# Performance work log

Hardware: AMD Instinct MI355X
Metric: run time of the kernel (lower is better)

Reference implementation:

```python
import jax, jax.numpy as jnp
import numpy as np

B, L, DIM = 4, 2048, 256
NSETS, PP, POSP, LTMP = 4, 4, 16, 16
PI = float(np.pi)


def setup_inputs() -> dict:
    key = jax.random.key(0)
    ks = jax.random.split(key, 8)
    d = DIM
    return {
        "x": jax.random.normal(ks[0], (B, L, d), jnp.float32),
        "key_proj": jax.random.normal(ks[1], (d, NSETS * PP), jnp.float32) / np.sqrt(d),
        "query_proj": jax.random.normal(ks[2], (d, NSETS * PP), jnp.float32) / np.sqrt(d),
        "ltm_key_proj": jax.random.normal(ks[3], (3 * d, LTMP), jnp.float32) / np.sqrt(3 * d),
        "pos_freqs": jnp.exp(jnp.arange(POSP, dtype=jnp.float32) * (-np.log(10000.0) / POSP)),
        "w_value": jax.random.normal(ks[4], (d, d), jnp.float32) / np.sqrt(d),
        "b_value": jnp.zeros(d, jnp.float32),
        "w_ltm_val": jax.random.normal(ks[5], (d, d), jnp.float32) / np.sqrt(d),
        "b_ltm_val": jnp.zeros(d, jnp.float32),
        "ln_gamma": jnp.ones(d, jnp.float32),
        "ln_beta": jnp.zeros(d, jnp.float32),
        "w_out": jax.random.normal(ks[6], (d, d), jnp.float32) / np.sqrt(d),
        "b_out": jnp.zeros(d, jnp.float32),
        "set_weights": jnp.ones(NSETS, jnp.float32),
        "pos_weight": jnp.ones(1, jnp.float32),
        "surprise_scale": jnp.array(5.0, jnp.float32),
        "surprise_bias": jnp.array(0.0, jnp.float32),
        "resonance_scale": jnp.array(5.0, jnp.float32),
        "resonance_threshold": jnp.array(0.3, jnp.float32),
        "ltm_weight": jnp.array(0.5, jnp.float32),
        "ltm_binding_memory": jnp.zeros((LTMP, d), jnp.complex64),
        "ltm_count": jnp.array(0.0, jnp.float32),
    }


def reference(x, key_proj, query_proj, ltm_key_proj, pos_freqs, w_value, b_value,
              w_ltm_val, b_ltm_val, ln_gamma, ln_beta, w_out, b_out, set_weights,
              pos_weight, surprise_scale, surprise_bias, resonance_scale,
              resonance_threshold, ltm_weight, ltm_binding_memory, ltm_count):
    Bx, Lx, D = x.shape
    # phasor encodings
    key_ph = jnp.exp(1j * (jnp.tanh(x @ key_proj) * PI)).reshape(Bx, Lx, NSETS, PP)
    qry_ph = jnp.exp(1j * (jnp.tanh(x @ query_proj) * PI)).reshape(Bx, Lx, NSETS, PP)
    V_real = x @ w_value + b_value
    weights = jax.nn.softmax(set_weights)
    # joint (cross-bank) phasors
    jk = jnp.prod(key_ph, axis=2)   # [B,L,PP]
    jq = jnp.prod(qry_ph, axis=2)
    # exclusive cumsum of joint keys -> resonance-based surprise write gate
    km = jnp.concatenate([jnp.zeros_like(jk[:, :1]), jnp.cumsum(jk[:, :-1], axis=1)], axis=1)
    rmag = jnp.abs(km * jnp.conj(jq)).mean(-1, keepdims=True)
    posf = jnp.maximum(jnp.arange(Lx, dtype=jnp.float32), 1.0)
    nres = rmag / jnp.sqrt(posf)[None, :, None]
    sc = jnp.clip(resonance_scale, 1.0, 20.0)
    th = jnp.clip(resonance_threshold, 0.1, 0.9)
    surprise = 0.5 * (1.0 - jnp.tanh(sc * (nres - th)))
    gate = jax.nn.sigmoid(surprise_scale * (surprise - 0.5) + surprise_bias)
    Vg = (V_real * gate).astype(jnp.complex64)
    # cross-bank holographic memory (joint key binding)
    cross = jnp.real((jnp.cumsum(jk[..., None] * Vg[:, :, None, :], axis=1)
                      * jnp.conj(jq)[..., None]).sum(2))
    # per-bank holographic memory over all planes
    bound_all = key_ph[..., None] * Vg[:, :, None, None, :]            # [B,L,S,P,D]
    mem_all = jnp.cumsum(bound_all.reshape(Bx, Lx, NSETS * PP, D), axis=1)
    mem_all = mem_all.reshape(Bx, Lx, NSETS, PP, D)
    per_bank = jnp.real((mem_all * jnp.conj(qry_ph)[..., None]).sum(3))  # [B,L,S,D]
    total = (per_bank * weights[None, None, :, None]).sum(2)
    total = (total + cross) / (NSETS + 1.0)
    # positional phasor memory (ungated V)
    pos_ph = jnp.exp(1j * (jnp.arange(Lx, dtype=jnp.float32)[:, None] * pos_freqs * 2.0 * PI))  # [L,P]
    Vc = V_real.astype(jnp.complex64)
    ret_pos = jnp.real((jnp.cumsum(pos_ph[None, :, :, None] * Vc[:, :, None, :], axis=1)
                        * jnp.conj(pos_ph)[None, :, :, None]).sum(2))
    total = 0.5 * total + 0.5 * (jax.nn.sigmoid(pos_weight) * ret_pos)  # fixed_gate = 0.5
    # LTM retrieval from persistent binding memory (detached buffers)
    p1 = jnp.arange(1, Lx + 1, dtype=jnp.float32)[None, :, None]
    rm = jnp.cumsum(x, axis=1) / p1
    rv = jnp.cumsum(x * x, axis=1) / p1 - rm * rm
    rs = jnp.sqrt(jnp.clip(rv, 1e-8, None))
    ltm_ph = jnp.exp(1j * (jnp.tanh(jnp.concatenate([x, rm, rs], -1) @ ltm_key_proj) * PI))  # [B,L,LTMP]
    pers = jnp.real((ltm_binding_memory[None, None] * jnp.conj(ltm_ph)[..., None]).sum(2))
    pnorm = jnp.sqrt(jnp.maximum(ltm_count, 1.0) * LTMP)
    total = total + jax.nn.sigmoid(ltm_weight) * (pers / pnorm)
    # output: LayerNorm + Linear on normalized retrieval, residual
    nrm = jnp.sqrt(jnp.arange(1, Lx + 1, dtype=jnp.float32) * PP)[None, :, None]
    h = total / nrm
    mu = h.mean(-1, keepdims=True)
    var = ((h - mu) ** 2).mean(-1, keepdims=True)
    hn = (h - mu) / jnp.sqrt(var + 1e-5) * ln_gamma + ln_beta
    return x + hn @ w_out + b_out
```

## Files before the change

kernel.cpp:

```cpp
#include <hip/hip_runtime.h>
#include <math.h>

#define B 4
#define L 2048
#define D 256
#define POSP 16
#define LTMP 16
#define T 64
#define C 32
#define F 72
#define PI_F 3.14159274101257324f
#define TWO_PI_D 6.283185307179586476925286766559

__global__ __launch_bounds__(256) void pos_kernel(const float* __restrict__ pos_freqs,
                                                  const float* __restrict__ lkp,
                                                  float* __restrict__ posc,
                                                  float* __restrict__ poss,
                                                  float* __restrict__ Wt) {
    int idx = blockIdx.x * 256 + threadIdx.x;
    if (idx < L * POSP) {
        int t = idx >> 4, p = idx & 15;
        float a = (float)t * pos_freqs[p];
        float th = (a * 2.0f) * PI_F;
        double r = fmod((double)th, TWO_PI_D);
        posc[idx] = (float)cos(r);
        poss[idx] = (float)sin(r);
    } else {
        int i2 = idx - L * POSP;
        if (i2 < 16 * 768) {
            int p = i2 / 768, j = i2 - p * 768;
            Wt[i2] = lkp[j * 16 + p];
        }
    }
}

__global__ __launch_bounds__(256) void featurize_kernel(
    const float* __restrict__ x, const float* __restrict__ key_proj,
    const float* __restrict__ query_proj, const float* __restrict__ w_value,
    const float* __restrict__ b_value, const float* __restrict__ set_weights,
    float* __restrict__ V, float* __restrict__ fk, float* __restrict__ fq,
    float* __restrict__ partial) {
    int cg = blockIdx.x;
    int rc = blockIdx.y;
    int b  = blockIdx.z;
    int row0 = rc * 64;
    int tid = threadIdx.x;
    __shared__ float xs[2][32][74];
    __shared__ float ws[2][32][84];
    __shared__ float zbuf[64][20];
    __shared__ float jkv[64][9];
    const bool has_proj = (cg < 2);
    const float* proj = (cg == 0) ? key_proj : query_proj;
    int rg = tid >> 4, cgi = tid & 15;
    int r0 = rg * 4, c0 = cgi * 4;
    int prow = tid >> 2, pc4 = tid & 3;
    float acc[4][4], accp[4];
#pragma unroll
    for (int i = 0; i < 4; i++) {
#pragma unroll
        for (int e = 0; e < 4; e++) acc[i][e] = 0.f;
        accp[i] = 0.f;
    }
    int rrA = tid >> 3, k4A = tid & 7;
    int jA = tid >> 4, c4A = tid & 15;
    float4 xr0, xr1, wr0, wr1, prr;

#define ISSUE_LOADS(kb_)                                                            \
    {                                                                               \
        xr0 = *(const float4*)(x + ((size_t)(b * L + row0 + rrA)) * D + (kb_) + k4A * 4);      \
        xr1 = *(const float4*)(x + ((size_t)(b * L + row0 + 32 + rrA)) * D + (kb_) + k4A * 4); \
        wr0 = *(const float4*)(w_value + (size_t)((kb_) + jA) * D + cg * 64 + c4A * 4);        \
        wr1 = *(const float4*)(w_value + (size_t)((kb_) + 16 + jA) * D + cg * 64 + c4A * 4);   \
        if (has_proj && tid < 128)                                                  \
            prr = *(const float4*)(proj + (size_t)((kb_) + (tid >> 2)) * 16 + (tid & 3) * 4);  \
    }
#define WRITE_LDS(bi)                                                               \
    {                                                                               \
        const float* xp0 = (const float*)&xr0;                                      \
        const float* xp1 = (const float*)&xr1;                                      \
        _Pragma("unroll")                                                           \
        for (int u = 0; u < 4; u++) {                                               \
            xs[bi][k4A * 4 + u][rrA] = xp0[u];                                      \
            xs[bi][k4A * 4 + u][32 + rrA] = xp1[u];                                 \
        }                                                                           \
        *(float4*)&ws[bi][jA][c4A * 4] = wr0;                                       \
        *(float4*)&ws[bi][16 + jA][c4A * 4] = wr1;                                  \
        if (has_proj && tid < 128)                                                  \
            *(float4*)&ws[bi][tid >> 2][64 + (tid & 3) * 4] = prr;                  \
    }

    ISSUE_LOADS(0);
    WRITE_LDS(0);
    __syncthreads();
    for (int kc = 0; kc < 8; kc++) {
        if (kc < 7) ISSUE_LOADS((kc + 1) * 32);
        int bi = kc & 1;
#pragma unroll 8
        for (int j = 0; j < 32; j++) {
            float2 xlo = *(float2*)&xs[bi][j][r0];
            float2 xhi = *(float2*)&xs[bi][j][r0 + 2];
            float4 wv = *(float4*)&ws[bi][j][c0];
            acc[0][0] += xlo.x * wv.x; acc[0][1] += xlo.x * wv.y; acc[0][2] += xlo.x * wv.z; acc[0][3] += xlo.x * wv.w;
            acc[1][0] += xlo.y * wv.x; acc[1][1] += xlo.y * wv.y; acc[1][2] += xlo.y * wv.z; acc[1][3] += xlo.y * wv.w;
            acc[2][0] += xhi.x * wv.x; acc[2][1] += xhi.x * wv.y; acc[2][2] += xhi.x * wv.z; acc[2][3] += xhi.x * wv.w;
            acc[3][0] += xhi.y * wv.x; acc[3][1] += xhi.y * wv.y; acc[3][2] += xhi.y * wv.z; acc[3][3] += xhi.y * wv.w;
            if (has_proj) {
                float xp = xs[bi][j][prow];
                float4 wp = *(float4*)&ws[bi][j][64 + pc4 * 4];
                accp[0] += xp * wp.x; accp[1] += xp * wp.y;
                accp[2] += xp * wp.z; accp[3] += xp * wp.w;
            }
        }
        if (kc < 7) WRITE_LDS((kc + 1) & 1);
        __syncthreads();
    }
#undef ISSUE_LOADS
#undef WRITE_LDS

    {
        int d0 = cg * 64 + c0;
        float4 bv = *(const float4*)(b_value + d0);
#pragma unroll
        for (int i = 0; i < 4; i++) {
            size_t o = ((size_t)(b * L + row0 + r0 + i)) * D + d0;
            *(float4*)(V + o) = make_float4(acc[i][0] + bv.x, acc[i][1] + bv.y,
                                            acc[i][2] + bv.z, acc[i][3] + bv.w);
        }
    }
    if (!has_proj) return;
#pragma unroll
    for (int e = 0; e < 4; e++) zbuf[prow][pc4 * 4 + e] = tanhf(accp[e]) * PI_F;
    __syncthreads();
    {
        int tt = tid >> 2, q = tid & 3;
        size_t bt = (size_t)(b * L + row0 + tt);
        if (cg == 0) {
            float* fp = fk + bt * 40;
#pragma unroll
            for (int e = 0; e < 4; e++) {
                int col = q * 4 + e;
                float si, co; sincosf(zbuf[tt][col], &si, &co);
                fp[2 * col] = co; fp[2 * col + 1] = si;
            }
            float zs = zbuf[tt][q] + zbuf[tt][4 + q] + zbuf[tt][8 + q] + zbuf[tt][12 + q];
            float si, co; sincosf(zs, &si, &co);
            fp[32 + 2 * q] = co; fp[33 + 2 * q] = si;
            jkv[tt][2 * q] = co; jkv[tt][2 * q + 1] = si;
        } else {
            float sw0 = set_weights[0], sw1 = set_weights[1], sw2 = set_weights[2], sw3 = set_weights[3];
            float mx = fmaxf(fmaxf(sw0, sw1), fmaxf(sw2, sw3));
            float e0 = expf(sw0 - mx), e1 = expf(sw1 - mx), e2 = expf(sw2 - mx), e3 = expf(sw3 - mx);
            float esum = e0 + e1 + e2 + e3;
            float wsoft[4] = {e0 / esum, e1 / esum, e2 / esum, e3 / esum};
            float* fp = fq + bt * 40;
#pragma unroll
            for (int e = 0; e < 4; e++) {
                int col = q * 4 + e;
                float si, co; sincosf(zbuf[tt][col], &si, &co);
                float sc = 0.1f * wsoft[col >> 2];
                fp[2 * col] = sc * co; fp[2 * col + 1] = sc * si;
            }
            float zs = zbuf[tt][q] + zbuf[tt][4 + q] + zbuf[tt][8 + q] + zbuf[tt][12 + q];
            float si, co; sincosf(zs, &si, &co);
            fp[32 + 2 * q] = 0.1f * co; fp[33 + 2 * q] = 0.1f * si;
        }
    }
    __syncthreads();
    if (cg == 0) {
        int h = tid >> 7, idxr = tid & 127;
        int rr2 = idxr >> 3, ch = idxr & 7;
#pragma unroll
        for (int s2 = 16; s2 >= 1; s2 >>= 1) {
            if (rr2 < s2) jkv[h * 32 + rr2][ch] += jkv[h * 32 + rr2 + s2][ch];
            __syncthreads();
        }
        if (rr2 == 0) partial[((size_t)(b * 64 + rc * 2 + h)) * 8 + ch] = jkv[h * 32][ch];
    }
}

__global__ __launch_bounds__(512) void gs_scan_kernel(const float* __restrict__ partial,
                                                      float* __restrict__ chunkoff) {
    int b = blockIdx.x;
    int tid = threadIdx.x;
    int c = tid >> 3, ch = tid & 7;
    __shared__ float sc_[64][9];
    float own = partial[((size_t)(b * 64 + c)) * 8 + ch];
    sc_[c][ch] = own;
    __syncthreads();
    for (int off = 1; off < 64; off <<= 1) {
        float v = 0.f;
        if (c >= off) v = sc_[c - off][ch];
        __syncthreads();
        if (c >= off) sc_[c][ch] += v;
        __syncthreads();
    }
    chunkoff[((size_t)(b * 64 + c)) * 8 + ch] = sc_[c][ch] - own;
}

__global__ __launch_bounds__(256) void gs_apply_kernel(
    float* __restrict__ fk, const float* __restrict__ chunkoff,
    const float* __restrict__ surprise_scale, const float* __restrict__ surprise_bias,
    const float* __restrict__ resonance_scale, const float* __restrict__ resonance_threshold) {
    int rc = blockIdx.x, b = blockIdx.y;
    int tid = threadIdx.x;
    int t = tid >> 3, ch = tid & 7;
    __shared__ float sc_[32][9];
    __shared__ float gbuf[32];
    float* fp = fk + ((size_t)(b * L + rc * 32 + t)) * 40;
    float own = fp[32 + ch];
    sc_[t][ch] = own;
    __syncthreads();
    for (int off = 1; off < 32; off <<= 1) {
        float v = 0.f;
        if (t >= off) v = sc_[t - off][ch];
        __syncthreads();
        if (t >= off) sc_[t][ch] += v;
        __syncthreads();
    }
    float run = chunkoff[((size_t)(b * 64 + rc)) * 8 + ch] + sc_[t][ch] - own;
    __syncthreads();
    sc_[t][ch] = run;
    __syncthreads();
    if (tid < 32) {
        int tg = rc * 32 + tid;
        float r0 = sc_[tid][0], r1 = sc_[tid][1], r2 = sc_[tid][2], r3 = sc_[tid][3];
        float r4 = sc_[tid][4], r5 = sc_[tid][5], r6 = sc_[tid][6], r7 = sc_[tid][7];
        float rmag = 0.25f * (sqrtf(r0 * r0 + r1 * r1) + sqrtf(r2 * r2 + r3 * r3) +
                              sqrtf(r4 * r4 + r5 * r5) + sqrtf(r6 * r6 + r7 * r7));
        float scv = fminf(fmaxf(resonance_scale[0], 1.f), 20.f);
        float thv = fminf(fmaxf(resonance_threshold[0], 0.1f), 0.9f);
        float nres = rmag / sqrtf(fmaxf((float)tg, 1.0f));
        float surprise = 0.5f * (1.0f - tanhf(scv * (nres - thv)));
        gbuf[tid] = 1.0f / (1.0f + expf(-(surprise_scale[0] * (surprise - 0.5f) + surprise_bias[0])));
    }
    __syncthreads();
    float gv = gbuf[t];
#pragma unroll
    for (int e = 0; e < 5; e++) fp[ch * 5 + e] *= gv;
}

__global__ __launch_bounds__(256) void stats16_kernel(const float* __restrict__ x,
                                                      float* __restrict__ Sx16,
                                                      float* __restrict__ Sxx16) {
    int s = blockIdx.x, b = blockIdx.y;
    int d = threadIdx.x;
    float sx = 0.f, sxx = 0.f;
#pragma unroll
    for (int k = 0; k < 16; k++) {
        float v = x[((size_t)(b * L + s * 16 + k)) * D + d];
        sx += v; sxx += v * v;
    }
    Sx16[((size_t)(b * 128 + s)) * D + d] = sx;
    Sxx16[((size_t)(b * 128 + s)) * D + d] = sxx;
}

__global__ __launch_bounds__(256) void ltm_z_kernel(
    const float* __restrict__ x, const float* __restrict__ Sx16,
    const float* __restrict__ Sxx16, const float* __restrict__ Wt,
    float* __restrict__ czsz) {
    int s = blockIdx.x, b = blockIdx.y;
    int tid = threadIdx.x;
    __shared__ float xs[16][260], rms[16][260], rss[16][260];
    float a0 = 0.f, a1 = 0.f, a2 = 0.f, a3 = 0.f;
    float c0 = 0.f, c1 = 0.f, c2 = 0.f, c3 = 0.f;
    int sp = 0;
    for (; sp + 4 <= s; sp += 4) {
        a0 += Sx16[((size_t)(b * 128 + sp)) * D + tid];
        a1 += Sx16[((size_t)(b * 128 + sp + 1)) * D + tid];
        a2 += Sx16[((size_t)(b * 128 + sp + 2)) * D + tid];
        a3 += Sx16[((size_t)(b * 128 + sp + 3)) * D + tid];
        c0 += Sxx16[((size_t)(b * 128 + sp)) * D + tid];
        c1 += Sxx16[((size_t)(b * 128 + sp + 1)) * D + tid];
        c2 += Sxx16[((size_t)(b * 128 + sp + 2)) * D + tid];
        c3 += Sxx16[((size_t)(b * 128 + sp + 3)) * D + tid];
    }
    for (; sp < s; sp++) {
        a0 += Sx16[((size_t)(b * 128 + sp)) * D + tid];
        c0 += Sxx16[((size_t)(b * 128 + sp)) * D + tid];
    }
    float runx = (a0 + a1) + (a2 + a3), runxx = (c0 + c1) + (c2 + c3);
    for (int k = 0; k < 16; k++) {
        int tg = s * 16 + k;
        float xv = x[((size_t)(b * L + tg)) * D + tid];
        runx += xv; runxx += xv * xv;
        float n = (float)(tg + 1);
        float rm = runx / n;
        float rv = runxx / n - rm * rm;
        xs[k][tid] = xv; rms[k][tid] = rm;
        rss[k][tid] = sqrtf(fmaxf(rv, 1e-8f));
    }
    __syncthreads();
    int tl = tid & 15, p = tid >> 4;
    const float* W0 = Wt + p * 768;
    float u0 = 0.f, u1 = 0.f, u2 = 0.f;
#pragma unroll 4
    for (int j4 = 0; j4 < 64; j4++) {
        float4 xv = *(float4*)&xs[tl][j4 * 4];
        float4 wx = *(const float4*)(W0 + j4 * 4);
        float4 rv = *(float4*)&rms[tl][j4 * 4];
        float4 wr = *(const float4*)(W0 + 256 + j4 * 4);
        float4 sv = *(float4*)&rss[tl][j4 * 4];
        float4 wz = *(const float4*)(W0 + 512 + j4 * 4);
        u0 += xv.x * wx.x + xv.y * wx.y + xv.z * wx.z + xv.w * wx.w;
        u1 += rv.x * wr.x + rv.y * wr.y + rv.z * wr.z + rv.w * wr.w;
        u2 += sv.x * wz.x + sv.y * wz.y + sv.z * wz.z + sv.w * wz.w;
    }
    float z = tanhf(u0 + u1 + u2) * PI_F;
    float si, co; sincosf(z, &si, &co);
    int tg = s * 16 + tl;
    czsz[((size_t)(b * L + tg)) * 32 + p] = co;
    czsz[((size_t)(b * L + tg)) * 32 + 16 + p] = si;
}

__global__ __launch_bounds__(256) void outer_sums_kernel(
    const float* __restrict__ V, const float* __restrict__ fk,
    const float* __restrict__ posc, const float* __restrict__ poss,
    float* __restrict__ Sh) {
    int g = blockIdx.x >> 1, h = blockIdx.x & 1;
    int c = blockIdx.y;
    int b = blockIdx.z;
    int tid = threadIdx.x;
    __shared__ float Fk[32][40];
    int F0 = g * 36;
    {
        int t = tid >> 3, q = tid & 7;
        int tg = c * T + h * 32 + t;
#pragma unroll
        for (int e = 0; e < 5; e++) {
            int fl = q * 5 + e;
            float v = 0.f;
            if (fl < 36) {
                int Fi = F0 + fl;
                if (Fi < 40) v = fk[((size_t)(b * L + tg)) * 40 + Fi];
                else {
                    int pf = Fi - 40;
                    v = (pf & 1) ? poss[tg * POSP + (pf >> 1)] : posc[tg * POSP + (pf >> 1)];
                }
            }
            Fk[t][fl] = v;
        }
    }
    __syncthreads();
    float acc[36];
#pragma unroll
    for (int f = 0; f < 36; f++) acc[f] = 0.f;
    for (int t = 0; t < 32; t++) {
        float v = V[((size_t)(b * L + c * T + h * 32 + t)) * D + tid];
#pragma unroll
        for (int f4 = 0; f4 < 9; f4++) {
            float4 fkv = *(float4*)&Fk[t][f4 * 4];
            acc[f4 * 4 + 0] += fkv.x * v;
            acc[f4 * 4 + 1] += fkv.y * v;
            acc[f4 * 4 + 2] += fkv.z * v;
            acc[f4 * 4 + 3] += fkv.w * v;
        }
    }
    for (int f = 0; f < 36; f++)
        Sh[((((size_t)(b * C + c)) * 2 + h) * F + F0 + f) * D + tid] = acc[f];
}

__global__ __launch_bounds__(256) void prefix_kernel(const float* __restrict__ Sh,
                                                     float* __restrict__ S) {
    int bf = blockIdx.x;
    int b = bf / F, f = bf % F;
    int d = threadIdx.x;
    float v0[C], v1[C];
#pragma unroll
    for (int c = 0; c < C; c++) {
        v0[c] = Sh[((((size_t)(b * C + c)) * 2 + 0) * F + f) * D + d];
        v1[c] = Sh[((((size_t)(b * C + c)) * 2 + 1) * F + f) * D + d];
    }
    float run = 0.f;
#pragma unroll
    for (int c = 0; c < C; c++) {
        S[(((size_t)(b * C + c)) * F + f) * D + d] = run;
        run += v0[c] + v1[c];
    }
}

__global__ __launch_bounds__(256) void intra_kernel(
    const float* __restrict__ V, float* __restrict__ ret,
    const float* __restrict__ fk, const float* __restrict__ fq,
    const float* __restrict__ posc, const float* __restrict__ poss,
    const float* __restrict__ Mexc, const float* __restrict__ pos_weight) {
    int tg = blockIdx.x >> 1, dh = blockIdx.x & 1;
    int c = blockIdx.y, b = blockIdx.z;
    int tid = threadIdx.x;
    int t0 = tg * 16;
    __shared__ float Fk[64][76];
    __shared__ float Fq[16][76];
    __shared__ float As[16][68];
    float posq = 0.5f / (1.0f + expf(-pos_weight[0]));
#pragma unroll
    for (int e = 0; e < 18; e++) {
        int idx = e * 256 + tid;
        int r = idx / 72, f = idx - r * 72;
        int tgl = c * T + r;
        float v;
        if (f < 40) v = fk[((size_t)(b * L + tgl)) * 40 + f];
        else { int pf = f - 40; v = (pf & 1) ? poss[tgl * POSP + (pf >> 1)] : posc[tgl * POSP + (pf >> 1)]; }
        Fk[r][f] = v;
    }
#pragma unroll
    for (int e = 0; e < 5; e++) {
        int idx = e * 256 + tid;
        if (idx < 1152) {
            int r = idx / 72, f = idx - r * 72;
            int tgl = c * T + t0 + r;
            float v;
            if (f < 40) v = fq[((size_t)(b * L + tgl)) * 40 + f];
            else { int pf = f - 40; v = posq * ((pf & 1) ? poss[tgl * POSP + (pf >> 1)] : posc[tgl * POSP + (pf >> 1)]); }
            Fq[r][f] = v;
        }
    }
    __syncthreads();
    {
        int r = tid >> 4, k0 = (tid & 15) * 4;
        int tglob = t0 + r;
#pragma unroll
        for (int j = 0; j < 4; j++) {
            int k = k0 + j;
            float a = 0.f;
            if (k <= tglob) {
#pragma unroll
                for (int f4 = 0; f4 < 18; f4++) {
                    float4 q = *(float4*)&Fq[r][f4 * 4];
                    float4 kk = *(float4*)&Fk[k][f4 * 4];
                    a += q.x * kk.x + q.y * kk.y + q.z * kk.z + q.w * kk.w;
                }
            }
            As[r][k] = a;
        }
    }
    __syncthreads();
    int dl = tid & 127, rowg = tid >> 7;
    int d = dh * 128 + dl;
    int r0 = rowg * 8;
    float acc[8];
#pragma unroll
    for (int i = 0; i < 8; i++) acc[i] = 0.f;
    const float* Mp = Mexc + (((size_t)(b * C + c)) * F) * D + d;
#pragma unroll 8
    for (int f = 0; f < F; f++) {
        float m = Mp[(size_t)f * D];
#pragma unroll
        for (int i = 0; i < 8; i++) acc[i] += Fq[r0 + i][f] * m;
    }
    const float* Vp = V + ((size_t)(b * L + c * T)) * D + d;
    int kmax = t0 + 16;
#pragma unroll 8
    for (int k = 0; k < kmax; k++) {
        float v = Vp[(size_t)k * D];
#pragma unroll
        for (int i = 0; i < 8; i++) acc[i] += As[r0 + i][k] * v;
    }
    float* Rp = ret + ((size_t)(b * L + c * T + t0 + r0)) * D + d;
#pragma unroll
    for (int i = 0; i < 8; i++) Rp[(size_t)i * D] = acc[i];
}

__global__ __launch_bounds__(256) void hprep_kernel(
    const float* __restrict__ retp, const float* __restrict__ czsz,
    const float* __restrict__ ltm_mem, const float* __restrict__ ltm_count,
    const float* __restrict__ ltm_weight, const float* __restrict__ ln_gamma,
    const float* __restrict__ ln_beta, float* __restrict__ hn) {
    int rc = blockIdx.x;
    int b  = blockIdx.y;
    int row0 = rc * 16;
    int tid = threadIdx.x;
    __shared__ float hb[16][260];
    __shared__ float cs[16][33];
    __shared__ float part1[16][17], part2[16][17];
    __shared__ float mu[16], rsig[16];
    float lsig = 1.f / (1.f + expf(-ltm_weight[0]));
    float pnorm = sqrtf(fmaxf(ltm_count[0], 1.f) * (float)LTMP);
    float lcoef = lsig / pnorm;
    float Mre[16], Mim[16];
#pragma unroll
    for (int p = 0; p < 16; p++) {
        Mre[p] = ltm_mem[(p * D + tid) * 2];
        Mim[p] = ltm_mem[(p * D + tid) * 2 + 1];
    }
    float gam = ln_gamma[tid], bet = ln_beta[tid];
#pragma unroll
    for (int e = 0; e < 2; e++) {
        int idx = e * 256 + tid;
        int t = idx >> 5, q = idx & 31;
        cs[t][q] = czsz[((size_t)(b * L + row0 + t)) * 32 + q];
    }
    __syncthreads();
#pragma unroll 4
    for (int t = 0; t < 16; t++) {
        int tg = row0 + t;
        float pers = 0.f;
#pragma unroll
        for (int p = 0; p < 16; p++) pers += Mre[p] * cs[t][p] + Mim[p] * cs[t][16 + p];
        float rv = retp[((size_t)(b * L + tg)) * D + tid];
        hb[t][tid] = (rv + lcoef * pers) / (2.0f * sqrtf((float)(tg + 1)));
    }
    __syncthreads();
    {
        int row = tid & 15, e = tid >> 4;
        float s1 = 0.f, s2 = 0.f;
#pragma unroll
        for (int k = 0; k < 16; k++) {
            float v = hb[row][e + 16 * k];
            s1 += v; s2 += v * v;
        }
        part1[row][e] = s1; part2[row][e] = s2;
    }
    __syncthreads();
    if (tid < 16) {
        float s1 = 0.f, s2 = 0.f;
#pragma unroll
        for (int e = 0; e < 16; e++) { s1 += part1[tid][e]; s2 += part2[tid][e]; }
        float m = s1 / 256.f;
        mu[tid] = m;
        rsig[tid] = rsqrtf(fmaxf(s2 / 256.f - m * m, 0.f) + 1e-5f);
    }
    __syncthreads();
#pragma unroll 4
    for (int t = 0; t < 16; t++)
        hn[((size_t)(b * L + row0 + t)) * D + tid] =
            (hb[t][tid] - mu[t]) * rsig[t] * gam + bet;
}

__global__ __launch_bounds__(256) void gemm_out_kernel(
    const float* __restrict__ hn, const float* __restrict__ w_out,
    const float* __restrict__ b_out, const float* __restrict__ x,
    float* __restrict__ out) {
    int cg = blockIdx.x;
    int rc = blockIdx.y;
    int b  = blockIdx.z;
    int row0 = rc * 64;
    int tid = threadIdx.x;
    __shared__ float hs[2][32][74];
    __shared__ float wo[2][32][68];
    int rg = tid >> 4, cgi = tid & 15;
    int r0 = rg * 4, c0 = cgi * 4;
    float acc[4][4];
#pragma unroll
    for (int i = 0; i < 4; i++)
#pragma unroll
        for (int e = 0; e < 4; e++) acc[i][e] = 0.f;
    int rrA = tid >> 3, k4A = tid & 7;
    int jA = tid >> 4, c4A = tid & 15;
    float4 hr0, hr1, wr0, wr1;

#define ISSUE_LOADS(kb_)                                                            \
    {                                                                               \
        hr0 = *(const float4*)(hn + ((size_t)(b * L + row0 + rrA)) * D + (kb_) + k4A * 4);      \
        hr1 = *(const float4*)(hn + ((size_t)(b * L + row0 + 32 + rrA)) * D + (kb_) + k4A * 4); \
        wr0 = *(const float4*)(w_out + (size_t)((kb_) + jA) * D + cg * 64 + c4A * 4);           \
        wr1 = *(const float4*)(w_out + (size_t)((kb_) + 16 + jA) * D + cg * 64 + c4A * 4);      \
    }
#define WRITE_LDS(bi)                                                               \
    {                                                                               \
        const float* hp0 = (const float*)&hr0;                                      \
        const float* hp1 = (const float*)&hr1;                                      \
        _Pragma("unroll")                                                           \
        for (int u = 0; u < 4; u++) {                                               \
            hs[bi][k4A * 4 + u][rrA] = hp0[u];                                      \
            hs[bi][k4A * 4 + u][32 + rrA] = hp1[u];                                 \
        }                                                                           \
        *(float4*)&wo[bi][jA][c4A * 4] = wr0;                                       \
        *(float4*)&wo[bi][16 + jA][c4A * 4] = wr1;                                  \
    }

    ISSUE_LOADS(0);
    WRITE_LDS(0);
    __syncthreads();
    for (int kc = 0; kc < 8; kc++) {
        if (kc < 7) ISSUE_LOADS((kc + 1) * 32);
        int bi = kc & 1;
#pragma unroll 8
        for (int j = 0; j < 32; j++) {
            float2 xlo = *(float2*)&hs[bi][j][r0];
            float2 xhi = *(float2*)&hs[bi][j][r0 + 2];
            float4 wv = *(float4*)&wo[bi][j][c0];
            acc[0][0] += xlo.x * wv.x; acc[0][1] += xlo.x * wv.y; acc[0][2] += xlo.x * wv.z; acc[0][3] += xlo.x * wv.w;
            acc[1][0] += xlo.y * wv.x; acc[1][1] += xlo.y * wv.y; acc[1][2] += xlo.y * wv.z; acc[1][3] += xlo.y * wv.w;
            acc[2][0] += xhi.x * wv.x; acc[2][1] += xhi.x * wv.y; acc[2][2] += xhi.x * wv.z; acc[2][3] += xhi.x * wv.w;
            acc[3][0] += xhi.y * wv.x; acc[3][1] += xhi.y * wv.y; acc[3][2] += xhi.y * wv.z; acc[3][3] += xhi.y * wv.w;
        }
        if (kc < 7) WRITE_LDS((kc + 1) & 1);
        __syncthreads();
    }
#undef ISSUE_LOADS
#undef WRITE_LDS
    {
        int d0 = cg * 64 + c0;
        float4 bo = *(const float4*)(b_out + d0);
#pragma unroll
        for (int i = 0; i < 4; i++) {
            size_t o = ((size_t)(b * L + row0 + r0 + i)) * D + d0;
            float4 xa = *(const float4*)(x + o);
            *(float4*)(out + o) = make_float4(xa.x + acc[i][0] + bo.x, xa.y + acc[i][1] + bo.y,
                                              xa.z + acc[i][2] + bo.z, xa.w + acc[i][3] + bo.w);
        }
    }
}

extern "C" void kernel_launch(void* const* d_in, const int* in_sizes, int n_in,
                              void* d_out, int out_size, void* d_ws, size_t ws_size,
                              hipStream_t stream) {
    (void)in_sizes; (void)n_in; (void)out_size; (void)ws_size;
    const float* x            = (const float*)d_in[0];
    const float* key_proj     = (const float*)d_in[1];
    const float* query_proj   = (const float*)d_in[2];
    const float* ltm_key_proj = (const float*)d_in[3];
    const float* pos_freqs    = (const float*)d_in[4];
    const float* w_value      = (const float*)d_in[5];
    const float* b_value      = (const float*)d_in[6];
    const float* ln_gamma     = (const float*)d_in[9];
    const float* ln_beta      = (const float*)d_in[10];
    const float* w_out        = (const float*)d_in[11];
    const float* b_out        = (const float*)d_in[12];
    const float* set_weights  = (const float*)d_in[13];
    const float* pos_weight   = (const float*)d_in[14];
    const float* surprise_scale      = (const float*)d_in[15];
    const float* surprise_bias       = (const float*)d_in[16];
    const float* resonance_scale     = (const float*)d_in[17];
    const float* resonance_threshold = (const float*)d_in[18];
    const float* ltm_weight   = (const float*)d_in[19];
    const float* ltm_mem      = (const float*)d_in[20];
    const float* ltm_count    = (const float*)d_in[21];
    float* out = (float*)d_out;

    float* ws = (float*)d_ws;
    size_t off = 0;
    float* V     = ws + off; off += (size_t)B * L * D;
    float* ret   = ws + off; off += (size_t)B * L * D;
    float* fk    = ws + off; off += (size_t)B * L * 40;
    float* fq    = ws + off; off += (size_t)B * L * 40;
    float* posc  = ws + off; off += (size_t)L * POSP;
    float* poss  = ws + off; off += (size_t)L * POSP;
    float* Sx16  = ws + off; off += (size_t)B * 128 * D;
    float* Sxx16 = ws + off; off += (size_t)B * 128 * D;
    float* czsz  = ws + off; off += (size_t)B * L * 32;
    float* Sh    = ws + off; off += (size_t)B * C * 2 * F * D;
    float* S     = ws + off; off += (size_t)B * C * F * D;
    float* partial  = ws + off; off += (size_t)B * 64 * 8;
    float* chunkoff = ws + off; off += (size_t)B * 64 * 8;
    float* Wt    = ws + off; off += (size_t)16 * 768;
    float* hn = V;

    pos_kernel<<<dim3(176), 256, 0, stream>>>(pos_freqs, ltm_key_proj, posc, poss, Wt);
    featurize_kernel<<<dim3(4, 32, B), 256, 0, stream>>>(x, key_proj, query_proj, w_value,
                                                         b_value, set_weights, V, fk, fq, partial);
    gs_scan_kernel<<<dim3(B), 512, 0, stream>>>(partial, chunkoff);
    gs_apply_kernel<<<dim3(64, B), 256, 0, stream>>>(fk, chunkoff, surprise_scale, surprise_bias,
                                                     resonance_scale, resonance_threshold);
    stats16_kernel<<<dim3(128, B), 256, 0, stream>>>(x, Sx16, Sxx16);
    ltm_z_kernel<<<dim3(128, B), 256, 0, stream>>>(x, Sx16, Sxx16, Wt, czsz);
    outer_sums_kernel<<<dim3(4, C, B), 256, 0, stream>>>(V, fk, posc, poss, Sh);
    prefix_kernel<<<dim3(B * F), 256, 0, stream>>>(Sh, S);
    intra_kernel<<<dim3(8, C, B), 256, 0, stream>>>(V, ret, fk, fq, posc, poss, S, pos_weight);
    hprep_kernel<<<dim3(128, B), 256, 0, stream>>>(ret, czsz, ltm_mem, ltm_count, ltm_weight,
                                                   ln_gamma, ln_beta, hn);
    gemm_out_kernel<<<dim3(4, 32, B), 256, 0, stream>>>(hn, w_out, b_out, x, out);
}
```

Measured before the change: 248.8 us.

## Fuse gate scan into one kernel and merge hprep LayerNorm into intra kernel

Replaces the three-step gated-surprise path (partial reduce in featurize, gs_scan, gs_apply) with a single 1024-thread-per-batch gate_kernel that scans joint key phasors across the whole sequence and rescales fk. Separately folds hprep (LTM retrieval, normalization, LayerNorm) into intra_kernel so each block computes all 256 channels for 16 rows, avoiding writing and re-reading the ret buffer. This removes two launches and a full B*L*D round trip. In exchange, intra now runs half as many blocks with 16 accumulators per thread, and the gate scan runs on only four blocks with a long serial log-step scan.

```diff
diff --git a/kernel.cpp b/kernel.cpp
--- a/kernel.cpp
+++ b/kernel.cpp
@@ -38,8 +38,7 @@
     const float* __restrict__ x, const float* __restrict__ key_proj,
     const float* __restrict__ query_proj, const float* __restrict__ w_value,
     const float* __restrict__ b_value, const float* __restrict__ set_weights,
-    float* __restrict__ V, float* __restrict__ fk, float* __restrict__ fq,
-    float* __restrict__ partial) {
+    float* __restrict__ V, float* __restrict__ fk, float* __restrict__ fq) {
     int cg = blockIdx.x;
     int rc = blockIdx.y;
     int b  = blockIdx.z;
@@ -48,7 +47,6 @@
     __shared__ float xs[2][32][74];
     __shared__ float ws[2][32][84];
     __shared__ float zbuf[64][20];
-    __shared__ float jkv[64][9];
     const bool has_proj = (cg < 2);
     const float* proj = (cg == 0) ? key_proj : query_proj;
     int rg = tid >> 4, cgi = tid & 15;
@@ -145,7 +143,6 @@
             float zs = zbuf[tt][q] + zbuf[tt][4 + q] + zbuf[tt][8 + q] + zbuf[tt][12 + q];
             float si, co; sincosf(zs, &si, &co);
             fp[32 + 2 * q] = co; fp[33 + 2 * q] = si;
-            jkv[tt][2 * q] = co; jkv[tt][2 * q + 1] = si;
         } else {
             float sw0 = set_weights[0], sw1 = set_weights[1], sw2 = set_weights[2], sw3 = set_weights[3];
             float mx = fmaxf(fmaxf(sw0, sw1), fmaxf(sw2, sw3));
@@ -165,78 +162,61 @@
             fp[32 + 2 * q] = 0.1f * co; fp[33 + 2 * q] = 0.1f * si;
         }
     }
-    __syncthreads();
-    if (cg == 0) {
-        int h = tid >> 7, idxr = tid & 127;
-        int rr2 = idxr >> 3, ch = idxr & 7;
-#pragma unroll
-        for (int s2 = 16; s2 >= 1; s2 >>= 1) {
-            if (rr2 < s2) jkv[h * 32 + rr2][ch] += jkv[h * 32 + rr2 + s2][ch];
-            __syncthreads();
-        }
-        if (rr2 == 0) partial[((size_t)(b * 64 + rc * 2 + h)) * 8 + ch] = jkv[h * 32][ch];
-    }
-}
-
-__global__ __launch_bounds__(512) void gs_scan_kernel(const float* __restrict__ partial,
-                                                      float* __restrict__ chunkoff) {
+}
+
+__global__ __launch_bounds__(1024) void gate_kernel(
+    float* __restrict__ fk,
+    const float* __restrict__ surprise_scale, const float* __restrict__ surprise_bias,
+    const float* __restrict__ resonance_scale, const float* __restrict__ resonance_threshold) {
     int b = blockIdx.x;
     int tid = threadIdx.x;
-    int c = tid >> 3, ch = tid & 7;
-    __shared__ float sc_[64][9];
-    float own = partial[((size_t)(b * 64 + c)) * 8 + ch];
-    sc_[c][ch] = own;
-    __syncthreads();
-    for (int off = 1; off < 64; off <<= 1) {
-        float v = 0.f;
-        if (c >= off) v = sc_[c - off][ch];
+    __shared__ float scan[1024][8];
+    float j0[8], j1[8], tot[8];
+    float* fp0 = fk + ((size_t)(b * L + tid * 2)) * 40;
+    float* fp1 = fk + ((size_t)(b * L + tid * 2 + 1)) * 40;
+#pragma unroll
+    for (int q = 0; q < 8; q++) {
+        j0[q] = fp0[32 + q];
+        j1[q] = fp1[32 + q];
+        tot[q] = j0[q] + j1[q];
+        scan[tid][q] = tot[q];
+    }
+    __syncthreads();
+    for (int off = 1; off < 1024; off <<= 1) {
+        float tmp[8];
+        if (tid >= off) {
+#pragma unroll
+            for (int q = 0; q < 8; q++) tmp[q] = scan[tid - off][q];
+        }
         __syncthreads();
-        if (c >= off) sc_[c][ch] += v;
+        if (tid >= off) {
+#pragma unroll
+            for (int q = 0; q < 8; q++) scan[tid][q] += tmp[q];
+        }
         __syncthreads();
     }
-    chunkoff[((size_t)(b * 64 + c)) * 8 + ch] = sc_[c][ch] - own;
-}
-
-__global__ __launch_bounds__(256) void gs_apply_kernel(
-    float* __restrict__ fk, const float* __restrict__ chunkoff,
-    const float* __restrict__ surprise_scale, const float* __restrict__ surprise_bias,
-    const float* __restrict__ resonance_scale, const float* __restrict__ resonance_threshold) {
-    int rc = blockIdx.x, b = blockIdx.y;
-    int tid = threadIdx.x;
-    int t = tid >> 3, ch = tid & 7;
-    __shared__ float sc_[32][9];
-    __shared__ float gbuf[32];
-    float* fp = fk + ((size_t)(b * L + rc * 32 + t)) * 40;
-    float own = fp[32 + ch];
-    sc_[t][ch] = own;
-    __syncthreads();
-    for (int off = 1; off < 32; off <<= 1) {
-        float v = 0.f;
-        if (t >= off) v = sc_[t - off][ch];
-        __syncthreads();
-        if (t >= off) sc_[t][ch] += v;
-        __syncthreads();
-    }
-    float run = chunkoff[((size_t)(b * 64 + rc)) * 8 + ch] + sc_[t][ch] - own;
-    __syncthreads();
-    sc_[t][ch] = run;
-    __syncthreads();
-    if (tid < 32) {
-        int tg = rc * 32 + tid;
-        float r0 = sc_[tid][0], r1 = sc_[tid][1], r2 = sc_[tid][2], r3 = sc_[tid][3];
-        float r4 = sc_[tid][4], r5 = sc_[tid][5], r6 = sc_[tid][6], r7 = sc_[tid][7];
-        float rmag = 0.25f * (sqrtf(r0 * r0 + r1 * r1) + sqrtf(r2 * r2 + r3 * r3) +
-                              sqrtf(r4 * r4 + r5 * r5) + sqrtf(r6 * r6 + r7 * r7));
-        float scv = fminf(fmaxf(resonance_scale[0], 1.f), 20.f);
-        float thv = fminf(fmaxf(resonance_threshold[0], 0.1f), 0.9f);
-        float nres = rmag / sqrtf(fmaxf((float)tg, 1.0f));
+    float run[8];
+#pragma unroll
+    for (int q = 0; q < 8; q++) run[q] = scan[tid][q] - tot[q];
+    float ss = surprise_scale[0], sb = surprise_bias[0];
+    float scv = fminf(fmaxf(resonance_scale[0], 1.f), 20.f);
+    float thv = fminf(fmaxf(resonance_threshold[0], 0.1f), 0.9f);
+#pragma unroll
+    for (int k = 0; k < 2; k++) {
+        int t = tid * 2 + k;
+        float* fp = k ? fp1 : fp0;
+        float rmag = 0.25f * (sqrtf(run[0] * run[0] + run[1] * run[1]) +
+                              sqrtf(run[2] * run[2] + run[3] * run[3]) +
+                              sqrtf(run[4] * run[4] + run[5] * run[5]) +
+                              sqrtf(run[6] * run[6] + run[7] * run[7]));
+        float nres = rmag / sqrtf(fmaxf((float)t, 1.0f));
         float surprise = 0.5f * (1.0f - tanhf(scv * (nres - thv)));
-        gbuf[tid] = 1.0f / (1.0f + expf(-(surprise_scale[0] * (surprise - 0.5f) + surprise_bias[0])));
-    }
-    __syncthreads();
-    float gv = gbuf[t];
-#pragma unroll
-    for (int e = 0; e < 5; e++) fp[ch * 5 + e] *= gv;
+        float gate = 1.0f / (1.0f + expf(-(ss * (surprise - 0.5f) + sb)));
+#pragma unroll
+        for (int q = 0; q < 8; q++) run[q] += (k ? j1[q] : j0[q]);
+#pragma unroll
+        for (int q = 0; q < 40; q++) fp[q] *= gate;
+    }
 }
 
 __global__ __launch_bounds__(256) void stats16_kernel(const float* __restrict__ x,
@@ -379,17 +359,26 @@
 }
 
 __global__ __launch_bounds__(256) void intra_kernel(
-    const float* __restrict__ V, float* __restrict__ ret,
+    const float* __restrict__ V, float* __restrict__ hn,
     const float* __restrict__ fk, const float* __restrict__ fq,
     const float* __restrict__ posc, const float* __restrict__ poss,
-    const float* __restrict__ Mexc, const float* __restrict__ pos_weight) {
-    int tg = blockIdx.x >> 1, dh = blockIdx.x & 1;
-    int c = blockIdx.y, b = blockIdx.z;
+    const float* __restrict__ Mexc, const float* __restrict__ pos_weight,
+    const float* __restrict__ czsz, const float* __restrict__ ltm_mem,
+    const float* __restrict__ ltm_count, const float* __restrict__ ltm_weight,
+    const float* __restrict__ ln_gamma, const float* __restrict__ ln_beta) {
+    int tg = blockIdx.x, c = blockIdx.y, b = blockIdx.z;
     int tid = threadIdx.x;
     int t0 = tg * 16;
-    __shared__ float Fk[64][76];
-    __shared__ float Fq[16][76];
-    __shared__ float As[16][68];
+    __shared__ float smem[8384];
+    float (*Fk)[76] = (float(*)[76])smem;
+    float (*Fq)[76] = (float(*)[76])(smem + 4864);
+    float (*As)[68] = (float(*)[68])(smem + 6080);
+    float (*cs)[33]  = (float(*)[33])(smem + 7168);
+    float (*part1)[17] = (float(*)[17])(smem + 7696);
+    float (*part2)[17] = (float(*)[17])(smem + 7968);
+    float* mu   = smem + 8240;
+    float* rsig = smem + 8256;
+    float (*hb)[260] = (float(*)[260])smem;
     float posq = 0.5f / (1.0f + expf(-pos_weight[0]));
 #pragma unroll
     for (int e = 0; e < 18; e++) {
@@ -413,6 +402,15 @@
             Fq[r][f] = v;
         }
     }
+    {
+        int idx2 = tid;
+#pragma unroll
+        for (int e = 0; e < 2; e++) {
+            int idx = e * 256 + idx2;
+            int t = idx >> 5, q = idx & 31;
+            cs[t][q] = czsz[((size_t)(b * L + c * T + t0 + t)) * 32 + q];
+        }
+    }
     __syncthreads();
     {
         int r = tid >> 4, k0 = (tid & 15) * 4;
@@ -433,18 +431,16 @@
         }
     }
     __syncthreads();
-    int dl = tid & 127, rowg = tid >> 7;
-    int d = dh * 128 + dl;
-    int r0 = rowg * 8;
-    float acc[8];
-#pragma unroll
-    for (int i = 0; i < 8; i++) acc[i] = 0.f;
+    int d = tid;
+    float acc[16];
+#pragma unroll
+    for (int i = 0; i < 16; i++) acc[i] = 0.f;
     const float* Mp = Mexc + (((size_t)(b * C + c)) * F) * D + d;
 #pragma unroll 8
     for (int f = 0; f < F; f++) {
         float m = Mp[(size_t)f * D];
 #pragma unroll
-        for (int i = 0; i < 8; i++) acc[i] += Fq[r0 + i][f] * m;
+        for (int i = 0; i < 16; i++) acc[i] += Fq[i][f] * m;
     }
     const float* Vp = V + ((size_t)(b * L + c * T)) * D + d;
     int kmax = t0 + 16;
@@ -452,52 +448,28 @@
     for (int k = 0; k < kmax; k++) {
         float v = Vp[(size_t)k * D];
 #pragma unroll
-        for (int i = 0; i < 8; i++) acc[i] += As[r0 + i][k] * v;
-    }
-    float* Rp = ret + ((size_t)(b * L + c * T + t0 + r0)) * D + d;
-#pragma unroll
-    for (int i = 0; i < 8; i++) Rp[(size_t)i * D] = acc[i];
-}
-
-__global__ __launch_bounds__(256) void hprep_kernel(
-    const float* __restrict__ retp, const float* __restrict__ czsz,
-    const float* __restrict__ ltm_mem, const float* __restrict__ ltm_count,
-    const float* __restrict__ ltm_weight, const float* __restrict__ ln_gamma,
-    const float* __restrict__ ln_beta, float* __restrict__ hn) {
-    int rc = blockIdx.x;
-    int b  = blockIdx.y;
-    int row0 = rc * 16;
-    int tid = threadIdx.x;
-    __shared__ float hb[16][260];
-    __shared__ float cs[16][33];
-    __shared__ float part1[16][17], part2[16][17];
-    __shared__ float mu[16], rsig[16];
+        for (int i = 0; i < 16; i++) acc[i] += As[i][k] * v;
+    }
     float lsig = 1.f / (1.f + expf(-ltm_weight[0]));
     float pnorm = sqrtf(fmaxf(ltm_count[0], 1.f) * (float)LTMP);
     float lcoef = lsig / pnorm;
     float Mre[16], Mim[16];
 #pragma unroll
     for (int p = 0; p < 16; p++) {
-        Mre[p] = ltm_mem[(p * D + tid) * 2];
-        Mim[p] = ltm_mem[(p * D + tid) * 2 + 1];
-    }
-    float gam = ln_gamma[tid], bet = ln_beta[tid];
-#pragma unroll
-    for (int e = 0; e < 2; e++) {
-        int idx = e * 256 + tid;
-        int t = idx >> 5, q = idx & 31;
-        cs[t][q] = czsz[((size_t)(b * L + row0 + t)) * 32 + q];
-    }
-    __syncthreads();
-#pragma unroll 4
-    for (int t = 0; t < 16; t++) {
-        int tg = row0 + t;
+        Mre[p] = ltm_mem[(p * D + d) * 2];
+        Mim[p] = ltm_mem[(p * D + d) * 2 + 1];
+    }
+#pragma unroll
+    for (int i = 0; i < 16; i++) {
         float pers = 0.f;
 #pragma unroll
-        for (int p = 0; p < 16; p++) pers += Mre[p] * cs[t][p] + Mim[p] * cs[t][16 + p];
-        float rv = retp[((size_t)(b * L + tg)) * D + tid];
-        hb[t][tid] = (rv + lcoef * pers) / (2.0f * sqrtf((float)(tg + 1)));
-    }
+        for (int p = 0; p < 16; p++) pers += Mre[p] * cs[i][p] + Mim[p] * cs[i][16 + p];
+        int tgl = c * T + t0 + i;
+        acc[i] = (acc[i] + lcoef * pers) / (2.0f * sqrtf((float)(tgl + 1)));
+    }
+    __syncthreads();
+#pragma unroll
+    for (int i = 0; i < 16; i++) hb[i][d] = acc[i];
     __syncthreads();
     {
         int row = tid & 15, e = tid >> 4;
@@ -519,10 +491,11 @@
         rsig[tid] = rsqrtf(fmaxf(s2 / 256.f - m * m, 0.f) + 1e-5f);
     }
     __syncthreads();
-#pragma unroll 4
-    for (int t = 0; t < 16; t++)
-        hn[((size_t)(b * L + row0 + t)) * D + tid] =
-            (hb[t][tid] - mu[t]) * rsig[t] * gam + bet;
+    float gam = ln_gamma[d], bet = ln_beta[d];
+#pragma unroll
+    for (int i = 0; i < 16; i++)
+        hn[((size_t)(b * L + c * T + t0 + i)) * D + d] =
+            (acc[i] - mu[i]) * rsig[i] * gam + bet;
 }
 
 __global__ __launch_bounds__(256) void gemm_out_kernel(
@@ -630,7 +603,7 @@
     float* ws = (float*)d_ws;
     size_t off = 0;
     float* V     = ws + off; off += (size_t)B * L * D;
-    float* ret   = ws + off; off += (size_t)B * L * D;
+    float* hn    = ws + off; off += (size_t)B * L * D;
     float* fk    = ws + off; off += (size_t)B * L * 40;
     float* fq    = ws + off; off += (size_t)B * L * 40;
     float* posc  = ws + off; off += (size_t)L * POSP;
@@ -640,23 +613,19 @@
     float* czsz  = ws + off; off += (size_t)B * L * 32;
     float* Sh    = ws + off; off += (size_t)B * C * 2 * F * D;
     float* S     = ws + off; off += (size_t)B * C * F * D;
-    float* partial  = ws + off; off += (size_t)B * 64 * 8;
-    float* chunkoff = ws + off; off += (size_t)B * 64 * 8;
     float* Wt    = ws + off; off += (size_t)16 * 768;
-    float* hn = V;
 
     pos_kernel<<<dim3(176), 256, 0, stream>>>(pos_freqs, ltm_key_proj, posc, poss, Wt);
     featurize_kernel<<<dim3(4, 32, B), 256, 0, stream>>>(x, key_proj, query_proj, w_value,
-                                                         b_value, set_weights, V, fk, fq, partial);
-    gs_scan_kernel<<<dim3(B), 512, 0, stream>>>(partial, chunkoff);
-    gs_apply_kernel<<<dim3(64, B), 256, 0, stream>>>(fk, chunkoff, surprise_scale, surprise_bias,
-                                                     resonance_scale, resonance_threshold);
+                                                         b_value, set_weights, V, fk, fq);
+    gate_kernel<<<dim3(B), 1024, 0, stream>>>(fk, surprise_scale, surprise_bias,
+                                              resonance_scale, resonance_threshold);
     stats16_kernel<<<dim3(128, B), 256, 0, stream>>>(x, Sx16, Sxx16);
     ltm_z_kernel<<<dim3(128, B), 256, 0, stream>>>(x, Sx16, Sxx16, Wt, czsz);
     outer_sums_kernel<<<dim3(4, C, B), 256, 0, stream>>>(V, fk, posc, poss, Sh);
     prefix_kernel<<<dim3(B * F), 256, 0, stream>>>(Sh, S);
-    intra_kernel<<<dim3(8, C, B), 256, 0, stream>>>(V, ret, fk, fq, posc, poss, S, pos_weight);
-    hprep_kernel<<<dim3(128, B), 256, 0, stream>>>(ret, czsz, ltm_mem, ltm_count, ltm_weight,
-                                                   ln_gamma, ln_beta, hn);
+    intra_kernel<<<dim3(4, C, B), 256, 0, stream>>>(V, hn, fk, fq, posc, poss, S, pos_weight,
+                                                    czsz, ltm_mem, ltm_count, ltm_weight,
+                                                    ln_gamma, ln_beta);
     gemm_out_kernel<<<dim3(4, 32, B), 256, 0, stream>>>(hn, w_out, b_out, x, out);
 }
```

Result: slower. 282.0 us (+13.3%).

## Interleave positional cos/sin, fuse stats into prep kernel, vectorize feature loads

Applied to the files above, without the earlier changes.

Positional cos/sin tables are stored interleaved per timestep so outer_sums and intra kernels can fill their shared feature tiles with float4 loads instead of per-element branching. The stats16 kernel is merged into the prep kernel, removing one launch. The intra score computation now computes four key dot products per thread unconditionally and applies the causal mask afterwards. This writes one wider float4 row and trades some wasted FLOPs on masked entries for less branching.

```diff
diff --git a/kernel.cpp b/kernel.cpp
--- a/kernel.cpp
+++ b/kernel.cpp
@@ -12,25 +12,40 @@
 #define PI_F 3.14159274101257324f
 #define TWO_PI_D 6.283185307179586476925286766559
 
-__global__ __launch_bounds__(256) void pos_kernel(const float* __restrict__ pos_freqs,
-                                                  const float* __restrict__ lkp,
-                                                  float* __restrict__ posc,
-                                                  float* __restrict__ poss,
-                                                  float* __restrict__ Wt) {
-    int idx = blockIdx.x * 256 + threadIdx.x;
-    if (idx < L * POSP) {
+__global__ __launch_bounds__(256) void prep_kernel(const float* __restrict__ pos_freqs,
+                                                   const float* __restrict__ lkp,
+                                                   const float* __restrict__ x,
+                                                   float* __restrict__ posci,
+                                                   float* __restrict__ Wt,
+                                                   float* __restrict__ Sx16,
+                                                   float* __restrict__ Sxx16) {
+    int bid = blockIdx.x;
+    int tid = threadIdx.x;
+    if (bid < 128) {
+        int idx = bid * 256 + tid;
         int t = idx >> 4, p = idx & 15;
         float a = (float)t * pos_freqs[p];
         float th = (a * 2.0f) * PI_F;
         double r = fmod((double)th, TWO_PI_D);
-        posc[idx] = (float)cos(r);
-        poss[idx] = (float)sin(r);
-    } else {
-        int i2 = idx - L * POSP;
+        posci[t * 32 + 2 * p] = (float)cos(r);
+        posci[t * 32 + 2 * p + 1] = (float)sin(r);
+    } else if (bid < 176) {
+        int i2 = (bid - 128) * 256 + tid;
         if (i2 < 16 * 768) {
             int p = i2 / 768, j = i2 - p * 768;
             Wt[i2] = lkp[j * 16 + p];
         }
+    } else {
+        int sb = bid - 176;
+        int s = sb & 127, b = sb >> 7;
+        float sx = 0.f, sxx = 0.f;
+#pragma unroll
+        for (int k = 0; k < 16; k++) {
+            float v = x[((size_t)(b * L + s * 16 + k)) * D + tid];
+            sx += v; sxx += v * v;
+        }
+        Sx16[((size_t)(b * 128 + s)) * D + tid] = sx;
+        Sxx16[((size_t)(b * 128 + s)) * D + tid] = sxx;
     }
 }
 
@@ -239,21 +254,6 @@
     for (int e = 0; e < 5; e++) fp[ch * 5 + e] *= gv;
 }
 
-__global__ __launch_bounds__(256) void stats16_kernel(const float* __restrict__ x,
-                                                      float* __restrict__ Sx16,
-                                                      float* __restrict__ Sxx16) {
-    int s = blockIdx.x, b = blockIdx.y;
-    int d = threadIdx.x;
-    float sx = 0.f, sxx = 0.f;
-#pragma unroll
-    for (int k = 0; k < 16; k++) {
-        float v = x[((size_t)(b * L + s * 16 + k)) * D + d];
-        sx += v; sxx += v * v;
-    }
-    Sx16[((size_t)(b * 128 + s)) * D + d] = sx;
-    Sxx16[((size_t)(b * 128 + s)) * D + d] = sxx;
-}
-
 __global__ __launch_bounds__(256) void ltm_z_kernel(
     const float* __restrict__ x, const float* __restrict__ Sx16,
     const float* __restrict__ Sxx16, const float* __restrict__ Wt,
@@ -314,30 +314,24 @@
 
 __global__ __launch_bounds__(256) void outer_sums_kernel(
     const float* __restrict__ V, const float* __restrict__ fk,
-    const float* __restrict__ posc, const float* __restrict__ poss,
-    float* __restrict__ Sh) {
+    const float* __restrict__ posci, float* __restrict__ Sh) {
     int g = blockIdx.x >> 1, h = blockIdx.x & 1;
     int c = blockIdx.y;
     int b = blockIdx.z;
     int tid = threadIdx.x;
     __shared__ float Fk[32][40];
     int F0 = g * 36;
-    {
-        int t = tid >> 3, q = tid & 7;
-        int tg = c * T + h * 32 + t;
-#pragma unroll
-        for (int e = 0; e < 5; e++) {
-            int fl = q * 5 + e;
-            float v = 0.f;
-            if (fl < 36) {
-                int Fi = F0 + fl;
-                if (Fi < 40) v = fk[((size_t)(b * L + tg)) * 40 + Fi];
-                else {
-                    int pf = Fi - 40;
-                    v = (pf & 1) ? poss[tg * POSP + (pf >> 1)] : posc[tg * POSP + (pf >> 1)];
-                }
-            }
-            Fk[t][fl] = v;
+#pragma unroll
+    for (int e = 0; e < 2; e++) {
+        int idx = e * 256 + tid;
+        if (idx < 288) {
+            int r = idx / 9, c4 = idx - r * 9;
+            int tg = c * T + h * 32 + r;
+            float4 v;
+            if (g == 0) v = *(const float4*)(fk + ((size_t)(b * L + tg)) * 40 + c4 * 4);
+            else if (c4 == 0) v = *(const float4*)(fk + ((size_t)(b * L + tg)) * 40 + 36);
+            else v = *(const float4*)(posci + tg * 32 + (c4 - 1) * 4);
+            *(float4*)&Fk[r][c4 * 4] = v;
         }
     }
     __syncthreads();
@@ -381,8 +375,8 @@
 __global__ __launch_bounds__(256) void intra_kernel(
     const float* __restrict__ V, float* __restrict__ ret,
     const float* __restrict__ fk, const float* __restrict__ fq,
-    const float* __restrict__ posc, const float* __restrict__ poss,
-    const float* __restrict__ Mexc, const float* __restrict__ pos_weight) {
+    const float* __restrict__ posci, const float* __restrict__ Mexc,
+    const float* __restrict__ pos_weight) {
     int tg = blockIdx.x >> 1, dh = blockIdx.x & 1;
     int c = blockIdx.y, b = blockIdx.z;
     int tid = threadIdx.x;
@@ -392,45 +386,52 @@
     __shared__ float As[16][68];
     float posq = 0.5f / (1.0f + expf(-pos_weight[0]));
 #pragma unroll
-    for (int e = 0; e < 18; e++) {
-        int idx = e * 256 + tid;
-        int r = idx / 72, f = idx - r * 72;
-        int tgl = c * T + r;
-        float v;
-        if (f < 40) v = fk[((size_t)(b * L + tgl)) * 40 + f];
-        else { int pf = f - 40; v = (pf & 1) ? poss[tgl * POSP + (pf >> 1)] : posc[tgl * POSP + (pf >> 1)]; }
-        Fk[r][f] = v;
-    }
-#pragma unroll
     for (int e = 0; e < 5; e++) {
         int idx = e * 256 + tid;
         if (idx < 1152) {
-            int r = idx / 72, f = idx - r * 72;
+            int r = idx / 18, c4 = idx - r * 18;
+            int tgl = c * T + r;
+            float4 v;
+            if (c4 < 10) v = *(const float4*)(fk + ((size_t)(b * L + tgl)) * 40 + c4 * 4);
+            else v = *(const float4*)(posci + tgl * 32 + (c4 - 10) * 4);
+            *(float4*)&Fk[r][c4 * 4] = v;
+        }
+    }
+#pragma unroll
+    for (int e = 0; e < 2; e++) {
+        int idx = e * 256 + tid;
+        if (idx < 288) {
+            int r = idx / 18, c4 = idx - r * 18;
             int tgl = c * T + t0 + r;
-            float v;
-            if (f < 40) v = fq[((size_t)(b * L + tgl)) * 40 + f];
-            else { int pf = f - 40; v = posq * ((pf & 1) ? poss[tgl * POSP + (pf >> 1)] : posc[tgl * POSP + (pf >> 1)]); }
-            Fq[r][f] = v;
+            float4 v;
+            if (c4 < 10) v = *(const float4*)(fq + ((size_t)(b * L + tgl)) * 40 + c4 * 4);
+            else {
+                v = *(const float4*)(posci + tgl * 32 + (c4 - 10) * 4);
+                v.x *= posq; v.y *= posq; v.z *= posq; v.w *= posq;
+            }
+            *(float4*)&Fq[r][c4 * 4] = v;
         }
     }
     __syncthreads();
     {
         int r = tid >> 4, k0 = (tid & 15) * 4;
         int tglob = t0 + r;
-#pragma unroll
-        for (int j = 0; j < 4; j++) {
-            int k = k0 + j;
-            float a = 0.f;
-            if (k <= tglob) {
-#pragma unroll
-                for (int f4 = 0; f4 < 18; f4++) {
-                    float4 q = *(float4*)&Fq[r][f4 * 4];
-                    float4 kk = *(float4*)&Fk[k][f4 * 4];
-                    a += q.x * kk.x + q.y * kk.y + q.z * kk.z + q.w * kk.w;
-                }
-            }
-            As[r][k] = a;
-        }
+        float a0 = 0.f, a1 = 0.f, a2 = 0.f, a3 = 0.f;
+#pragma unroll
+        for (int f4 = 0; f4 < 18; f4++) {
+            float4 q = *(float4*)&Fq[r][f4 * 4];
+            float4 k0v = *(float4*)&Fk[k0 + 0][f4 * 4];
+            float4 k1v = *(float4*)&Fk[k0 + 1][f4 * 4];
+            float4 k2v = *(float4*)&Fk[k0 + 2][f4 * 4];
+            float4 k3v = *(float4*)&Fk[k0 + 3][f4 * 4];
+            a0 += q.x * k0v.x + q.y * k0v.y + q.z * k0v.z + q.w * k0v.w;
+            a1 += q.x * k1v.x + q.y * k1v.y + q.z * k1v.z + q.w * k1v.w;
+            a2 += q.x * k2v.x + q.y * k2v.y + q.z * k2v.z + q.w * k2v.w;
+            a3 += q.x * k3v.x + q.y * k3v.y + q.z * k3v.z + q.w * k3v.w;
+        }
+        float4 av = make_float4((k0 + 0 <= tglob) ? a0 : 0.f, (k0 + 1 <= tglob) ? a1 : 0.f,
+                                (k0 + 2 <= tglob) ? a2 : 0.f, (k0 + 3 <= tglob) ? a3 : 0.f);
+        *(float4*)&As[tid >> 4][k0] = av;
     }
     __syncthreads();
     int dl = tid & 127, rowg = tid >> 7;
@@ -633,29 +634,28 @@
     float* ret   = ws + off; off += (size_t)B * L * D;
     float* fk    = ws + off; off += (size_t)B * L * 40;
     float* fq    = ws + off; off += (size_t)B * L * 40;
-    float* posc  = ws + off; off += (size_t)L * POSP;
-    float* poss  = ws + off; off += (size_t)L * POSP;
+    float* posci = ws + off; off += (size_t)L * 32;
     float* Sx16  = ws + off; off += (size_t)B * 128 * D;
     float* Sxx16 = ws + off; off += (size_t)B * 128 * D;
     float* czsz  = ws + off; off += (size_t)B * L * 32;
     float* Sh    = ws + off; off += (size_t)B * C * 2 * F * D;
     float* S     = ws + off; off += (size_t)B * C * F * D;
+    float* Wt    = ws + off; off += (size_t)16 * 768;
     float* partial  = ws + off; off += (size_t)B * 64 * 8;
     float* chunkoff = ws + off; off += (size_t)B * 64 * 8;
-    float* Wt    = ws + off; off += (size_t)16 * 768;
     float* hn = V;
 
-    pos_kernel<<<dim3(176), 256, 0, stream>>>(pos_freqs, ltm_key_proj, posc, poss, Wt);
+    prep_kernel<<<dim3(688), 256, 0, stream>>>(pos_freqs, ltm_key_proj, x, posci, Wt,
+                                               Sx16, Sxx16);
     featurize_kernel<<<dim3(4, 32, B), 256, 0, stream>>>(x, key_proj, query_proj, w_value,
                                                          b_value, set_weights, V, fk, fq, partial);
     gs_scan_kernel<<<dim3(B), 512, 0, stream>>>(partial, chunkoff);
     gs_apply_kernel<<<dim3(64, B), 256, 0, stream>>>(fk, chunkoff, surprise_scale, surprise_bias,
                                                      resonance_scale, resonance_threshold);
-    stats16_kernel<<<dim3(128, B), 256, 0, stream>>>(x, Sx16, Sxx16);
     ltm_z_kernel<<<dim3(128, B), 256, 0, stream>>>(x, Sx16, Sxx16, Wt, czsz);
-    outer_sums_kernel<<<dim3(4, C, B), 256, 0, stream>>>(V, fk, posc, poss, Sh);
+    outer_sums_kernel<<<dim3(4, C, B), 256, 0, stream>>>(V, fk, posci, Sh);
     prefix_kernel<<<dim3(B * F), 256, 0, stream>>>(Sh, S);
-    intra_kernel<<<dim3(8, C, B), 256, 0, stream>>>(V, ret, fk, fq, posc, poss, S, pos_weight);
+    intra_kernel<<<dim3(8, C, B), 256, 0, stream>>>(V, ret, fk, fq, posci, S, pos_weight);
     hprep_kernel<<<dim3(128, B), 256, 0, stream>>>(ret, czsz, ltm_mem, ltm_count, ltm_weight,
                                                    ln_gamma, ln_beta, hn);
     gemm_out_kernel<<<dim3(4, 32, B), 256, 0, stream>>>(hn, w_out, b_out, x, out);
```

After: 246.2 us. About the same (-1.1%).
